# Performance work log

Measured on AMD Instinct MI355X. Metric: run time of the kernel, lower is better.

## Reference

```python
import jax, jax.numpy as jnp
import numpy as np
from functools import partial

H = 768
E = 1536
B = 4
L = 4096

def layer_norm(x, g, b, eps=1e-5):
    mu = jnp.mean(x, axis=-1, keepdims=True)
    var = jnp.mean((x - mu) ** 2, axis=-1, keepdims=True)
    return (x - mu) * jax.lax.rsqrt(var + eps) * g + b

def l2_normalize(x, eps=1e-12):
    n = jnp.sqrt(jnp.sum(x * x, axis=-1, keepdims=True))
    return x / jnp.maximum(n, eps)

def dw_conv(x, w):
    # x: [B, L, E], w: [E, 1, 3] depthwise kernel (torch Conv1d groups=E layout)
    y = jax.lax.conv_general_dilated(
        x.transpose(0, 2, 1), w, window_strides=(1,), padding=[(1, 1)],
        dimension_numbers=('NCH', 'OIH', 'NCH'), feature_group_count=E)
    return y.transpose(0, 2, 1)

def setup_inputs() -> dict:
    key = jax.random.key(0)
    ks = jax.random.split(key, 12)
    d = {}
    d['x'] = jax.random.normal(ks[0], (B, L, H), jnp.float32)
    d['ln1_g'] = jnp.ones((H,), jnp.float32)
    d['ln1_b'] = jnp.zeros((H,), jnp.float32)
    d['ln2_g'] = jnp.ones((E,), jnp.float32)
    d['ln2_b'] = jnp.zeros((E,), jnp.float32)
    d['W_in'] = 0.02 * jax.random.normal(ks[1], (3 * E, H), jnp.float32)
    d['b_in'] = jnp.zeros((3 * E,), jnp.float32)
    d['W_beta'] = jnp.zeros((E, H), jnp.float32)  # torch init: constant 0
    d['b_beta'] = jnp.ones((E,), jnp.float32)     # torch init: constant 1
    d['W_out'] = 0.02 * jax.random.normal(ks[2], (H, E), jnp.float32)
    d['b_out'] = jnp.zeros((H,), jnp.float32)
    d['W1'] = 0.02 * jax.random.normal(ks[3], (4 * H, H), jnp.float32)
    d['b1'] = jnp.zeros((4 * H,), jnp.float32)
    d['W2'] = 0.02 * jax.random.normal(ks[4], (H, 4 * H), jnp.float32)
    d['b2'] = jnp.zeros((H,), jnp.float32)
    d['conv_w'] = jax.random.normal(ks[5], (E, 1, 3), jnp.float32) / jnp.sqrt(3.0)
    d['attn_scale'] = jnp.ones((1,), jnp.float32)
    return d

def reference(x, ln1_g, ln1_b, ln2_g, ln2_b, W_in, b_in, W_beta, b_beta,
              W_out, b_out, W1, b1, W2, b2, conv_w, attn_scale):
    shortcut = x
    xn = layer_norm(x, ln1_g, ln1_b)
    qkv = xn @ W_in.T + b_in
    q, k, v = jnp.split(qkv, 3, axis=-1)
    q = jax.nn.silu(q)
    k = jax.nn.silu(k)
    v = jax.nn.gelu(v, approximate=False)
    q = l2_normalize(q) + 0.1 * k
    k = l2_normalize(k) + 0.1 * q
    q = dw_conv(q, conv_w)
    k = dw_conv(k, conv_w)
    v = dw_conv(v, conv_w)
    beta = jax.nn.sigmoid(xn @ W_beta.T + b_beta) * 0.9 + 0.1
    # initial state is zero, so v_old = 0 and v_new = beta * v (same math as torch code)
    v_new = beta * v                                   # [B, L, E]
    state = jnp.einsum('ble,blf->bef', v_new, k)       # v_new^T @ k : [B, E, E]
    out = jnp.einsum('blf,bef->ble', q, state)         # q @ state^T
    out = out * attn_scale
    out = layer_norm(out, ln2_g, ln2_b)
    out = out @ W_out.T + b_out
    x = shortcut + out
    h = layer_norm(x, ln1_g, ln1_b)
    h = jax.nn.gelu(h @ W1.T + b1, approximate=False) @ W2.T + b2
    return x + h
```

## Files before the change

kernel.cpp:

```cpp
#include <hip/hip_runtime.h>
#include <hip/hip_bf16.h>
#include <cstdint>
#include <cstddef>

using bf16_t = __hip_bfloat16;
typedef __bf16 bf16x8 __attribute__((ext_vector_type(8)));
typedef __bf16 bf16x4 __attribute__((ext_vector_type(4)));
typedef float f32x4 __attribute__((ext_vector_type(4)));

#define DEVI static __device__ __forceinline__

DEVI float b2f(bf16_t v) { return __bfloat162float(v); }

DEVI float fsigmoid(float x) { return 1.0f / (1.0f + __expf(-x)); }
DEVI float fsilu(float x) { return x * fsigmoid(x); }

DEVI float ferf(float x) {
    const float ax = fabsf(x);
    const float t = 1.0f / fmaf(0.3275911f, ax, 1.0f);
    float p = fmaf(1.061405429f, t, -1.453152027f);
    p = fmaf(p, t, 1.421413741f);
    p = fmaf(p, t, -0.284496736f);
    p = fmaf(p, t, 0.254829592f);
    p = p * t * __expf(-ax * ax);
    return copysignf(1.0f - p, x);
}
DEVI float fgelu(float x) { return 0.5f * x * (1.0f + ferf(x * 0.70710678118654752440f)); }

DEVI void g2l16(const bf16_t* g, bf16_t* l) {
    __builtin_amdgcn_global_load_lds(
        (const __attribute__((address_space(1))) void*)g,
        (__attribute__((address_space(3))) void*)l,
        16, 0, 0);
}

DEVI f32x4 mfma16(bf16x8 a, bf16x8 b, f32x4 c) {
    return __builtin_amdgcn_mfma_f32_16x16x32_bf16(a, b, c, 0, 0, 0);
}

template<int ACT, bool RESID, bool OUTBF, bool QKVSPLIT>
__global__ __launch_bounds__(256) void gemm_nt(
    const bf16_t* __restrict__ A, const bf16_t* __restrict__ B,
    void* __restrict__ Cout, const float* __restrict__ bias,
    const float* __restrict__ resid,
    float* __restrict__ normq, float* __restrict__ normk,
    int M, int N, int K, long long sA, long long sB, long long sC)
{
    __shared__ bf16_t As[128 * 64];
    __shared__ bf16_t Bs[128 * 64];

    const int t  = threadIdx.x;
    const int w  = t >> 6;
    const int ln = t & 63;
    const long long bz = blockIdx.z;
    A += bz * sA;
    B += bz * sB;
    const long long cbase = QKVSPLIT ? 0 : bz * sC;

    const int m0 = blockIdx.y * 128;
    const int n0 = blockIdx.x * 128;
    const int wm = (w >> 1) * 64;
    const int wn = (w & 1) * 64;

    f32x4 acc[4][4] = {};

    const int sr = ln >> 3;
    const int sc = (ln & 7) ^ sr;
    const bf16_t* Ap = A + (size_t)(m0 + w * 32 + sr) * K + sc * 8;
    const bf16_t* Bp = B + (size_t)(n0 + w * 32 + sr) * K + sc * 8;
    bf16_t* ldsA = &As[(w * 32) * 64];
    bf16_t* ldsB = &Bs[(w * 32) * 64];

    const int fr = ln & 15;
    const int qd = ln >> 4;
    int roA[4], roB[4];
#pragma unroll
    for (int i = 0; i < 4; ++i) {
        roA[i] = (wm + i * 16 + fr) * 64;
        roB[i] = (wn + i * 16 + fr) * 64;
    }
    const int so0 = ((qd)     ^ (fr & 7)) * 8;
    const int so1 = ((4 + qd) ^ (fr & 7)) * 8;

    for (int k0 = 0; k0 < K; k0 += 64) {
#pragma unroll
        for (int i = 0; i < 4; ++i) {
            g2l16(Ap + (size_t)(i * 8) * K, ldsA + (i * 8) * 64);
            g2l16(Bp + (size_t)(i * 8) * K, ldsB + (i * 8) * 64);
        }
        Ap += 64; Bp += 64;
        __syncthreads();

        bf16x8 af[4], bfr[4];
#pragma unroll
        for (int i = 0; i < 4; ++i) {
            af[i]  = *(const bf16x8*)&As[roA[i] + so0];
            bfr[i] = *(const bf16x8*)&Bs[roB[i] + so0];
        }
#pragma unroll
        for (int mi = 0; mi < 4; ++mi)
#pragma unroll
            for (int ni = 0; ni < 4; ++ni)
                acc[mi][ni] = mfma16(bfr[ni], af[mi], acc[mi][ni]);
#pragma unroll
        for (int i = 0; i < 4; ++i) {
            af[i]  = *(const bf16x8*)&As[roA[i] + so1];
            bfr[i] = *(const bf16x8*)&Bs[roB[i] + so1];
        }
#pragma unroll
        for (int mi = 0; mi < 4; ++mi)
#pragma unroll
            for (int ni = 0; ni < 4; ++ni)
                acc[mi][ni] = mfma16(bfr[ni], af[mi], acc[mi][ni]);
        __syncthreads();
    }

    const int rb = qd * 4;
    const int seg = QKVSPLIT ? (n0 / 1536) : 0;
    f32x4 bias4[4];
#pragma unroll
    for (int ni = 0; ni < 4; ++ni) {
        f32x4 z = {};
        bias4[ni] = bias ? *(const f32x4*)&bias[n0 + wn + ni * 16 + rb] : z;
    }
#pragma unroll
    for (int mi = 0; mi < 4; ++mi) {
        const int row = m0 + wm + mi * 16 + fr;
        float s2 = 0.f;
#pragma unroll
        for (int ni = 0; ni < 4; ++ni) {
            const int col0 = n0 + wn + ni * 16 + rb;
            f32x4 v = acc[mi][ni] + bias4[ni];
            if constexpr (ACT == 1) {
#pragma unroll
                for (int r = 0; r < 4; ++r) v[r] = fgelu(v[r]);
            }
            if constexpr (ACT == 3) {
                if (seg <= 1) {
#pragma unroll
                    for (int r = 0; r < 4; ++r) v[r] = fsilu(v[r]);
                    s2 += v[0]*v[0] + v[1]*v[1] + v[2]*v[2] + v[3]*v[3];
                } else if (seg == 2) {
#pragma unroll
                    for (int r = 0; r < 4; ++r) v[r] = fgelu(v[r]);
                } else {
#pragma unroll
                    for (int r = 0; r < 4; ++r) v[r] = fsigmoid(v[r]) * 0.9f + 0.1f;
                }
            }
            long long off;
            if constexpr (QKVSPLIT) {
                off = (long long)seg * sC + (long long)row * 1536
                    + (col0 - seg * 1536);
            } else {
                off = cbase + (long long)row * N + col0;
            }
            if constexpr (RESID) v += *(const f32x4*)&resid[off];
            if constexpr (OUTBF) {
                bf16x4 o;
#pragma unroll
                for (int r = 0; r < 4; ++r) o[r] = (__bf16)v[r];
                *(bf16x4*)((bf16_t*)Cout + off) = o;
            } else {
                *(f32x4*)((float*)Cout + off) = v;
            }
        }
        if constexpr (ACT == 3) {
            if (seg <= 1) {
                s2 += __shfl_xor(s2, 16, 64);
                s2 += __shfl_xor(s2, 32, 64);
                if (qd == 0)
                    atomicAdd((seg == 0 ? normq : normk) + row, s2);
            }
        }
    }
}

template<int ACT, bool RESID, bool OUTBF, bool QKVSPLIT>
__global__ __launch_bounds__(512) void gemm256(
    const bf16_t* __restrict__ A, const bf16_t* __restrict__ B,
    void* __restrict__ Cout, const float* __restrict__ bias,
    const float* __restrict__ resid,
    float* __restrict__ normq, float* __restrict__ normk,
    int M, int N, int K, long long sA, long long sB, long long sC)
{
    __shared__ bf16_t As[256 * 64];
    __shared__ bf16_t Bs[256 * 64];

    const int t  = threadIdx.x;
    const int w  = t >> 6;
    const int ln = t & 63;
    const int wr = w >> 2;
    const int wc = w & 3;
    const long long bz = blockIdx.z;
    A += bz * sA;
    B += bz * sB;
    const long long cbase = QKVSPLIT ? 0 : bz * sC;

    const int m0 = blockIdx.y * 256;
    const int n0 = blockIdx.x * 256;

    const int sr = ln >> 3;
    const int scx = ((ln & 7) ^ sr) * 8;
    const bf16_t* gA[2];
    const bf16_t* gB[2];
    int lA[2], lB[2];
#pragma unroll
    for (int i = 0; i < 2; ++i) {
        const int b  = w * 2 + i;
        const int rA = ((b >> 3) << 7) + ((b & 7) << 3);
        const int rB = ((b >> 2) << 6) + ((b & 3) << 3);
        gA[i] = A + (size_t)(m0 + rA + sr) * K + scx;
        gB[i] = B + (size_t)(n0 + rB + sr) * K + scx;
        lA[i] = rA * 64;
        lB[i] = rB * 64;
    }
    const size_t K64 = (size_t)K * 64;
    const size_t K32 = (size_t)K * 32;
    const int NT = K >> 6;

    const int fr = ln & 15;
    const int qd = ln >> 4;
    const int ck0 = ((qd)     ^ (fr & 7)) * 8;
    const int ck1 = ((4 + qd) ^ (fr & 7)) * 8;
    const int raB = (wr * 128 + fr) * 64;
    const int rbB = (wc * 64  + fr) * 64;

    f32x4 acc[8][4] = {};

#define STAGE_A0(kc) do { g2l16(gA[0] + (kc), &As[lA[0]]); \
                          g2l16(gA[1] + (kc), &As[lA[1]]); } while (0)
#define STAGE_A1(kc) do { g2l16(gA[0] + K64 + (kc), &As[lA[0] + 4096]); \
                          g2l16(gA[1] + K64 + (kc), &As[lA[1] + 4096]); } while (0)
#define STAGE_B0(kc) do { g2l16(gB[0] + (kc), &Bs[lB[0]]); \
                          g2l16(gB[1] + (kc), &Bs[lB[1]]); } while (0)
#define STAGE_B1(kc) do { g2l16(gB[0] + K32 + (kc), &Bs[lB[0] + 2048]); \
                          g2l16(gB[1] + K32 + (kc), &Bs[lB[1] + 2048]); } while (0)

    STAGE_A0(0);
    STAGE_B0(0);
    STAGE_B1(0);
    STAGE_A1(0);

    bf16x8 a0[4][2], a1[4][2], bq0[2][2], bq1[2][2];

    for (int u = 0; u < NT; ++u) {
        const size_t kc1 = (size_t)(u + 1) * 64;
        const bool p1 = (u + 1) < NT;

        asm volatile("s_waitcnt vmcnt(4)" ::: "memory");
        __builtin_amdgcn_sched_barrier(0);
        __builtin_amdgcn_s_barrier();
        __builtin_amdgcn_sched_barrier(0);
#pragma unroll
        for (int mi = 0; mi < 4; ++mi) {
            a0[mi][0] = *(const bf16x8*)&As[raB + mi * 1024 + ck0];
            a0[mi][1] = *(const bf16x8*)&As[raB + mi * 1024 + ck1];
        }
#pragma unroll
        for (int ni = 0; ni < 2; ++ni) {
            bq0[ni][0] = *(const bf16x8*)&Bs[rbB + ni * 1024 + ck0];
            bq0[ni][1] = *(const bf16x8*)&Bs[rbB + ni * 1024 + ck1];
        }
        asm volatile("s_waitcnt lgkmcnt(0)" ::: "memory");
        __builtin_amdgcn_sched_barrier(0);
        __builtin_amdgcn_s_setprio(1);
#pragma unroll
        for (int mi = 0; mi < 4; ++mi)
#pragma unroll
            for (int ni = 0; ni < 2; ++ni) {
                acc[mi][ni] = mfma16(bq0[ni][0], a0[mi][0], acc[mi][ni]);
                acc[mi][ni] = mfma16(bq0[ni][1], a0[mi][1], acc[mi][ni]);
            }
        __builtin_amdgcn_s_setprio(0);
        __builtin_amdgcn_sched_barrier(0);

        asm volatile("s_waitcnt vmcnt(2)" ::: "memory");
        __builtin_amdgcn_sched_barrier(0);
        __builtin_amdgcn_s_barrier();
        __builtin_amdgcn_sched_barrier(0);
        if (p1) STAGE_A0(kc1);
#pragma unroll
        for (int ni = 0; ni < 2; ++ni) {
            bq1[ni][0] = *(const bf16x8*)&Bs[rbB + 2048 + ni * 1024 + ck0];
            bq1[ni][1] = *(const bf16x8*)&Bs[rbB + 2048 + ni * 1024 + ck1];
        }
        asm volatile("s_waitcnt lgkmcnt(0)" ::: "memory");
        __builtin_amdgcn_sched_barrier(0);
        __builtin_amdgcn_s_setprio(1);
#pragma unroll
        for (int mi = 0; mi < 4; ++mi)
#pragma unroll
            for (int ni = 0; ni < 2; ++ni) {
                acc[mi][ni + 2] = mfma16(bq1[ni][0], a0[mi][0], acc[mi][ni + 2]);
                acc[mi][ni + 2] = mfma16(bq1[ni][1], a0[mi][1], acc[mi][ni + 2]);
            }
        __builtin_amdgcn_s_setprio(0);
        __builtin_amdgcn_sched_barrier(0);

        if (p1) asm volatile("s_waitcnt vmcnt(2)" ::: "memory");
        else    asm volatile("s_waitcnt vmcnt(0)" ::: "memory");
        __builtin_amdgcn_sched_barrier(0);
        __builtin_amdgcn_s_barrier();
        __builtin_amdgcn_sched_barrier(0);
        if (p1) { STAGE_B0(kc1); STAGE_B1(kc1); }
#pragma unroll
        for (int mi = 0; mi < 4; ++mi) {
            a1[mi][0] = *(const bf16x8*)&As[raB + 4096 + mi * 1024 + ck0];
            a1[mi][1] = *(const bf16x8*)&As[raB + 4096 + mi * 1024 + ck1];
        }
        asm volatile("s_waitcnt lgkmcnt(0)" ::: "memory");
        __builtin_amdgcn_sched_barrier(0);
        __builtin_amdgcn_s_setprio(1);
#pragma unroll
        for (int mi = 0; mi < 4; ++mi)
#pragma unroll
            for (int ni = 0; ni < 2; ++ni) {
                acc[mi + 4][ni] = mfma16(bq0[ni][0], a1[mi][0], acc[mi + 4][ni]);
                acc[mi + 4][ni] = mfma16(bq0[ni][1], a1[mi][1], acc[mi + 4][ni]);
            }
        __builtin_amdgcn_s_setprio(0);
        __builtin_amdgcn_sched_barrier(0);

        __builtin_amdgcn_s_barrier();
        __builtin_amdgcn_sched_barrier(0);
        if (p1) STAGE_A1(kc1);
        __builtin_amdgcn_s_setprio(1);
#pragma unroll
        for (int mi = 0; mi < 4; ++mi)
#pragma unroll
            for (int ni = 0; ni < 2; ++ni) {
                acc[mi + 4][ni + 2] = mfma16(bq1[ni][0], a1[mi][0], acc[mi + 4][ni + 2]);
                acc[mi + 4][ni + 2] = mfma16(bq1[ni][1], a1[mi][1], acc[mi + 4][ni + 2]);
            }
        __builtin_amdgcn_s_setprio(0);
        __builtin_amdgcn_sched_barrier(0);
    }
#undef STAGE_A0
#undef STAGE_A1
#undef STAGE_B0
#undef STAGE_B1

    const int rb = qd * 4;
    const int seg = QKVSPLIT ? (n0 / 1536) : 0;
    f32x4 bias4[4];
#pragma unroll
    for (int ni = 0; ni < 4; ++ni) {
        f32x4 z = {};
        bias4[ni] = bias ? *(const f32x4*)&bias[n0 + wc * 64 + ni * 16 + rb] : z;
    }
#pragma unroll
    for (int mi = 0; mi < 8; ++mi) {
        const int row = m0 + wr * 128 + mi * 16 + fr;
        float s2 = 0.f;
#pragma unroll
        for (int ni = 0; ni < 4; ++ni) {
            const int col0 = n0 + wc * 64 + ni * 16 + rb;
            f32x4 v = acc[mi][ni] + bias4[ni];
            if constexpr (ACT == 1) {
#pragma unroll
                for (int r = 0; r < 4; ++r) v[r] = fgelu(v[r]);
            }
            if constexpr (ACT == 3) {
                if (seg <= 1) {
#pragma unroll
                    for (int r = 0; r < 4; ++r) v[r] = fsilu(v[r]);
                    s2 += v[0]*v[0] + v[1]*v[1] + v[2]*v[2] + v[3]*v[3];
                } else if (seg == 2) {
#pragma unroll
                    for (int r = 0; r < 4; ++r) v[r] = fgelu(v[r]);
                } else {
#pragma unroll
                    for (int r = 0; r < 4; ++r) v[r] = fsigmoid(v[r]) * 0.9f + 0.1f;
                }
            }
            long long off;
            if constexpr (QKVSPLIT) {
                off = (long long)seg * sC + (long long)row * 1536
                    + (col0 - seg * 1536);
            } else {
                off = cbase + (long long)row * N + col0;
            }
            if constexpr (RESID) v += *(const f32x4*)&resid[off];
            if constexpr (OUTBF) {
                bf16x4 o;
#pragma unroll
                for (int r = 0; r < 4; ++r) o[r] = (__bf16)v[r];
                *(bf16x4*)((bf16_t*)Cout + off) = o;
            } else {
                *(f32x4*)((float*)Cout + off) = v;
            }
        }
        if constexpr (ACT == 3) {
            if (seg <= 1) {
                s2 += __shfl_xor(s2, 16, 64);
                s2 += __shfl_xor(s2, 32, 64);
                if (qd == 0)
                    atomicAdd((seg == 0 ? normq : normk) + row, s2);
            }
        }
    }
}

template<int NT>
__global__ __launch_bounds__(NT) void ln_v4(
    const float* __restrict__ x, const float* __restrict__ g,
    const float* __restrict__ b, bf16_t* __restrict__ out)
{
    constexpr int n = NT * 4;
    constexpr int NW = NT / 64;
    const int row = blockIdx.x, t = threadIdx.x;
    f32x4 v = *(const f32x4*)&x[(size_t)row * n + t * 4];
    float s  = v[0] + v[1] + v[2] + v[3];
    float ss = v[0]*v[0] + v[1]*v[1] + v[2]*v[2] + v[3]*v[3];
#pragma unroll
    for (int m = 32; m; m >>= 1) { s += __shfl_xor(s, m, 64); ss += __shfl_xor(ss, m, 64); }
    __shared__ float red[2 * NW];
    const int w = t >> 6;
    if ((t & 63) == 0) { red[w] = s; red[NW + w] = ss; }
    __syncthreads();
    s = 0.f; ss = 0.f;
#pragma unroll
    for (int i = 0; i < NW; ++i) { s += red[i]; ss += red[NW + i]; }
    const float mean = s / n;
    const float rstd = rsqrtf(ss / n - mean * mean + 1e-5f);
    const f32x4 gv = *(const f32x4*)&g[t * 4];
    const f32x4 bv = *(const f32x4*)&b[t * 4];
    bf16x4 o;
#pragma unroll
    for (int r = 0; r < 4; ++r)
        o[r] = (__bf16)((v[r] - mean) * rstd * gv[r] + bv[r]);
    *(bf16x4*)&out[(size_t)row * n + t * 4] = o;
}

__global__ __launch_bounds__(192) void ln_bf16_1536(
    const bf16_t* __restrict__ x, const float* __restrict__ g,
    const float* __restrict__ b, bf16_t* __restrict__ out,
    const float* __restrict__ scale_ptr)
{
    const int row = blockIdx.x, t = threadIdx.x;
    const float scale = scale_ptr[0];
    const bf16x8 x8 = *(const bf16x8*)&x[(size_t)row * 1536 + t * 8];
    float v[8];
    float s = 0.f, ss = 0.f;
#pragma unroll
    for (int i = 0; i < 8; ++i) {
        v[i] = (float)x8[i] * scale;
        s += v[i]; ss += v[i] * v[i];
    }
#pragma unroll
    for (int m = 32; m; m >>= 1) { s += __shfl_xor(s, m, 64); ss += __shfl_xor(ss, m, 64); }
    __shared__ float red[6];
    const int w = t >> 6;
    if ((t & 63) == 0) { red[w] = s; red[3 + w] = ss; }
    __syncthreads();
    s  = red[0] + red[1] + red[2];
    ss = red[3] + red[4] + red[5];
    const float mean = s / 1536.f;
    const float rstd = rsqrtf(ss / 1536.f - mean * mean + 1e-5f);
    const f32x4 g0 = *(const f32x4*)&g[t * 8];
    const f32x4 g1 = *(const f32x4*)&g[t * 8 + 4];
    const f32x4 b0 = *(const f32x4*)&b[t * 8];
    const f32x4 b1 = *(const f32x4*)&b[t * 8 + 4];
    bf16x8 o;
#pragma unroll
    for (int r = 0; r < 4; ++r) {
        o[r]     = (__bf16)((v[r]     - mean) * rstd * g0[r] + b0[r]);
        o[r + 4] = (__bf16)((v[r + 4] - mean) * rstd * g1[r] + b1[r]);
    }
    *(bf16x8*)&out[(size_t)row * 1536 + t * 8] = o;
}

__global__ __launch_bounds__(256) void ac_qk(
    const bf16_t* __restrict__ qs, const bf16_t* __restrict__ ks,
    const float* __restrict__ nq, const float* __restrict__ nk,
    bf16_t* __restrict__ qc, bf16_t* __restrict__ kT,
    const float* __restrict__ cw)
{
    constexpr int L = 4096, E = 1536;
    const int b = blockIdx.z;
    const int e0 = blockIdx.x * 64, l0 = blockIdx.y * 64;
    const int t = threadIdx.x;
    const int e = e0 + (t & 15) * 4;
    const int lbase = l0 + (t >> 4) * 4;
    const size_t rowL = (size_t)b * L;

    float w0[4], w1[4], w2[4];
#pragma unroll
    for (int i = 0; i < 4; ++i) {
        w0[i] = cw[(e + i) * 3 + 0];
        w1[i] = cw[(e + i) * 3 + 1];
        w2[i] = cw[(e + i) * 3 + 2];
    }

    float sq[6][4], sk[6][4];
#pragma unroll
    for (int j = 0; j < 6; ++j) {
        const int l = lbase - 1 + j;
        if (l < 0 || l >= L) {
#pragma unroll
            for (int i = 0; i < 4; ++i) { sq[j][i] = 0.f; sk[j][i] = 0.f; }
            continue;
        }
        const size_t off = (rowL + l) * E + e;
        const bf16x4 q4 = *(const bf16x4*)&qs[off];
        const bf16x4 k4 = *(const bf16x4*)&ks[off];
        const float rq = 1.0f / fmaxf(sqrtf(nq[rowL + l]), 1e-12f);
        const float rk = 1.0f / fmaxf(sqrtf(nk[rowL + l]), 1e-12f);
#pragma unroll
        for (int i = 0; i < 4; ++i) {
            const float q1 = (float)q4[i] * rq + 0.1f * (float)k4[i];
            const float k1 = (float)k4[i] * rk + 0.1f * q1;
            sq[j][i] = q1; sk[j][i] = k1;
        }
    }

#pragma unroll
    for (int j = 0; j < 4; ++j) {
        bf16x4 oq;
#pragma unroll
        for (int i = 0; i < 4; ++i)
            oq[i] = (__bf16)(w0[i] * sq[j][i] + w1[i] * sq[j + 1][i] + w2[i] * sq[j + 2][i]);
        *(bf16x4*)&qc[(rowL + lbase + j) * E + e] = oq;
    }
#pragma unroll
    for (int i = 0; i < 4; ++i) {
        bf16x4 ok;
#pragma unroll
        for (int j = 0; j < 4; ++j)
            ok[j] = (__bf16)(w0[i] * sk[j][i] + w1[i] * sk[j + 1][i] + w2[i] * sk[j + 2][i]);
        *(bf16x4*)&kT[((size_t)b * E + e + i) * L + lbase] = ok;
    }
}

__global__ __launch_bounds__(256) void ac_v(
    const bf16_t* __restrict__ vg, const bf16_t* __restrict__ beta,
    bf16_t* __restrict__ vT, const float* __restrict__ cw)
{
    constexpr int L = 4096, E = 1536;
    const int b = blockIdx.z;
    const int e0 = blockIdx.x * 64, l0 = blockIdx.y * 64;
    const int t = threadIdx.x;
    const int e = e0 + (t & 15) * 4;
    const int lbase = l0 + (t >> 4) * 4;
    const size_t rowL = (size_t)b * L;

    float w0[4], w1[4], w2[4];
#pragma unroll
    for (int i = 0; i < 4; ++i) {
        w0[i] = cw[(e + i) * 3 + 0];
        w1[i] = cw[(e + i) * 3 + 1];
        w2[i] = cw[(e + i) * 3 + 2];
    }

    float s[6][4];
#pragma unroll
    for (int j = 0; j < 6; ++j) {
        const int l = lbase - 1 + j;
        if (l < 0 || l >= L) {
#pragma unroll
            for (int i = 0; i < 4; ++i) s[j][i] = 0.f;
            continue;
        }
        const bf16x4 v4 = *(const bf16x4*)&vg[(rowL + l) * E + e];
#pragma unroll
        for (int i = 0; i < 4; ++i) s[j][i] = (float)v4[i];
    }

    float o[4][4];
#pragma unroll
    for (int j = 0; j < 4; ++j) {
        const bf16x4 b4 = *(const bf16x4*)&beta[(rowL + lbase + j) * E + e];
#pragma unroll
        for (int i = 0; i < 4; ++i)
            o[j][i] = (w0[i] * s[j][i] + w1[i] * s[j + 1][i] + w2[i] * s[j + 2][i])
                      * (float)b4[i];
    }
#pragma unroll
    for (int i = 0; i < 4; ++i) {
        bf16x4 ov;
#pragma unroll
        for (int j = 0; j < 4; ++j) ov[j] = (__bf16)o[j][i];
        *(bf16x4*)&vT[((size_t)b * E + e + i) * L + lbase] = ov;
    }
}

__global__ __launch_bounds__(256) void prep1(
    const float* __restrict__ Win, const float* __restrict__ Wbeta,
    const float* __restrict__ bin, const float* __restrict__ bbeta,
    bf16_t* __restrict__ Wcat, float* __restrict__ bcat)
{
    constexpr int nWin4 = 3 * 1536 * 768 / 4;
    constexpr int nWb4  = 1536 * 768 / 4;
    const int i = blockIdx.x * 256 + threadIdx.x;
    if (i < nWin4) {
        const f32x4 v = ((const f32x4*)Win)[i];
        bf16x4 o;
#pragma unroll
        for (int r = 0; r < 4; ++r) o[r] = (__bf16)v[r];
        ((bf16x4*)Wcat)[i] = o;
    } else if (i < nWin4 + nWb4) {
        const f32x4 v = ((const f32x4*)Wbeta)[i - nWin4];
        bf16x4 o;
#pragma unroll
        for (int r = 0; r < 4; ++r) o[r] = (__bf16)v[r];
        ((bf16x4*)Wcat)[i] = o;
    } else {
        const int j = i - nWin4 - nWb4;
        ((f32x4*)bcat)[j] = (j < 1152) ? ((const f32x4*)bin)[j]
                                       : ((const f32x4*)bbeta)[j - 1152];
    }
}

__global__ __launch_bounds__(256) void prep2(
    const float* __restrict__ Wout, const float* __restrict__ W1,
    const float* __restrict__ W2, bf16_t* __restrict__ dst)
{
    constexpr int n0 = 768 * 1536 / 4;
    constexpr int n1 = n0 + 3072 * 768 / 4;
    const int i = blockIdx.x * 256 + threadIdx.x;
    const float* src;
    int j;
    if (i < n0)      { src = Wout; j = i; }
    else if (i < n1) { src = W1;   j = i - n0; }
    else             { src = W2;   j = i - n1; }
    const f32x4 v = ((const f32x4*)src)[j];
    bf16x4 o;
#pragma unroll
    for (int r = 0; r < 4; ++r) o[r] = (__bf16)v[r];
    ((bf16x4*)dst)[i] = o;
}

__global__ void diag_ws(float* o, float v) { o[threadIdx.x] = v; }


extern "C" void kernel_launch(void* const* d_in, const int* in_sizes, int n_in,
                              void* d_out, int out_size, void* d_ws, size_t ws_size,
                              hipStream_t stream)
{
    constexpr int B = 4, L = 4096, H = 768, E = 1536;
    constexpr int T = B * L;
    constexpr size_t SEGE = (size_t)T * E;
    constexpr size_t S    = SEGE * 2;
    constexpr size_t o_bcat  = 5 * S;
    constexpr size_t o_norms = o_bcat + 6144 * 4;
    constexpr size_t WS_NEED = o_norms + (size_t)T * 8;

    const float* x       = (const float*)d_in[0];
    const float* ln1_g   = (const float*)d_in[1];
    const float* ln1_b   = (const float*)d_in[2];
    const float* ln2_g   = (const float*)d_in[3];
    const float* ln2_b   = (const float*)d_in[4];
    const float* W_in    = (const float*)d_in[5];
    const float* b_in    = (const float*)d_in[6];
    const float* W_beta  = (const float*)d_in[7];
    const float* b_beta  = (const float*)d_in[8];
    const float* W_out   = (const float*)d_in[9];
    const float* b_out   = (const float*)d_in[10];
    const float* W1      = (const float*)d_in[11];
    const float* b1      = (const float*)d_in[12];
    const float* W2      = (const float*)d_in[13];
    const float* b2      = (const float*)d_in[14];
    const float* conv_w  = (const float*)d_in[15];
    const float* attn_sc = (const float*)d_in[16];

    if (ws_size < WS_NEED) {
        diag_ws<<<1, 256, 0, stream>>>((float*)d_out,
                                       10000.0f + (float)(ws_size >> 20));
        return;
    }

    char* ws = (char*)d_ws;
    bf16_t* slotA = (bf16_t*)(ws + 0 * S);
    bf16_t* slotB = (bf16_t*)(ws + 1 * S);
    bf16_t* slotC = (bf16_t*)(ws + 2 * S);
    bf16_t* slotD = (bf16_t*)(ws + 3 * S);
    bf16_t* slotE = (bf16_t*)(ws + 4 * S);
    float*  bcat  = (float*)(ws + o_bcat);
    float*  nq    = (float*)(ws + o_norms);
    float*  nk    = nq + T;

    bf16_t* Wcat = slotE;
    bf16_t* xn   = (bf16_t*)((char*)slotE + (size_t)6144 * H * 2);

    bf16_t* vT    = slotE;
    bf16_t* kT    = slotC;
    bf16_t* qc    = slotD;
    bf16_t* state = slotA;
    bf16_t* WoutB = (bf16_t*)((char*)slotA + (size_t)20 * 1024 * 1024);
    bf16_t* W1B   = WoutB + (size_t)H * E;
    bf16_t* W2B   = W1B + (size_t)4 * H * H;
    bf16_t* attn  = slotB;
    bf16_t* ln2o  = slotE;
    float*  x2    = (float*)slotC;
    bf16_t* xn2   = slotB;
    bf16_t* h1    = slotD;

    hipMemsetAsync(nq, 0, (size_t)T * 2 * sizeof(float), stream);
    prep1<<<4614, 256, 0, stream>>>(W_in, W_beta, b_in, b_beta, Wcat, bcat);

    ln_v4<192><<<T, 192, 0, stream>>>(x, ln1_g, ln1_b, xn);

    gemm256<3, false, true, true><<<dim3(6144 / 256, T / 256, 1), 512, 0, stream>>>(
        xn, Wcat, slotA, bcat, nullptr, nq, nk, T, 6144, H, 0, 0, (long long)SEGE);

    ac_v <<<dim3(E / 64, L / 64, B), 256, 0, stream>>>(slotC, slotD, vT, conv_w);
    ac_qk<<<dim3(E / 64, L / 64, B), 256, 0, stream>>>(slotA, slotB, nq, nk, qc, kT, conv_w);

    prep2<<<5760, 256, 0, stream>>>(W_out, W1, W2, WoutB);

    gemm_nt<0, false, true, false><<<dim3(E / 128, E / 128, B), 256, 0, stream>>>(
        vT, kT, state, nullptr, nullptr, nullptr, nullptr, E, E, L,
        (long long)E * L, (long long)E * L, (long long)E * E);

    gemm256<0, false, true, false><<<dim3(E / 256, L / 256, B), 512, 0, stream>>>(
        qc, state, attn, nullptr, nullptr, nullptr, nullptr, L, E, E,
        (long long)L * E, (long long)E * E, (long long)L * E);

    ln_bf16_1536<<<T, 192, 0, stream>>>(attn, ln2_g, ln2_b, ln2o, attn_sc);

    gemm_nt<0, true, false, false><<<dim3(H / 128, T / 128, 1), 256, 0, stream>>>(
        ln2o, WoutB, x2, b_out, x, nullptr, nullptr, T, H, E, 0, 0, 0);

    ln_v4<192><<<T, 192, 0, stream>>>(x2, ln1_g, ln1_b, xn2);

    gemm256<1, false, true, false><<<dim3(4 * H / 256, T / 256, 1), 512, 0, stream>>>(
        xn2, W1B, h1, b1, nullptr, nullptr, nullptr, T, 4 * H, H, 0, 0, 0);

    gemm_nt<0, true, false, false><<<dim3(H / 128, T / 128, 1), 256, 0, stream>>>(
        h1, W2B, (float*)d_out, b2, x2, nullptr, nullptr, T, H, 4 * H, 0, 0, 0);
}
```

Measured before the change: 1.150 ms.

## Double-buffer LDS tiles in gemm256 with two-half k-step pipeline

Replaces the single-buffered four-phase staging schedule with ping-pong LDS buffers for A and B. The next tile's A loads are issued at the top of each iteration and its B loads are issued mid-iteration, while the current tile is consumed in two k-halves of 8x4 MFMAs each. The aim is to cut the number of workgroup barriers per k-step and overlap global-to-LDS copies with compute more fully. In exchange, LDS use doubles to 128KB, which may limit occupancy, and more fragment registers are live at once.

```diff
diff --git a/kernel.cpp b/kernel.cpp
--- a/kernel.cpp
+++ b/kernel.cpp
@@ -184,8 +184,8 @@
     float* __restrict__ normq, float* __restrict__ normk,
     int M, int N, int K, long long sA, long long sB, long long sC)
 {
-    __shared__ bf16_t As[256 * 64];
-    __shared__ bf16_t Bs[256 * 64];
+    __shared__ bf16_t As[2][256 * 64];
+    __shared__ bf16_t Bs[2][256 * 64];
 
     const int t  = threadIdx.x;
     const int w  = t >> 6;
@@ -223,123 +223,87 @@
     const int qd = ln >> 4;
     const int ck0 = ((qd)     ^ (fr & 7)) * 8;
     const int ck1 = ((4 + qd) ^ (fr & 7)) * 8;
-    const int raB = (wr * 128 + fr) * 64;
-    const int rbB = (wc * 64  + fr) * 64;
+    int roA[8], roB[4];
+#pragma unroll
+    for (int mi = 0; mi < 8; ++mi) roA[mi] = (wr * 128 + mi * 16 + fr) * 64;
+#pragma unroll
+    for (int ni = 0; ni < 4; ++ni) roB[ni] = (wc * 64 + ni * 16 + fr) * 64;
 
     f32x4 acc[8][4] = {};
 
-#define STAGE_A0(kc) do { g2l16(gA[0] + (kc), &As[lA[0]]); \
-                          g2l16(gA[1] + (kc), &As[lA[1]]); } while (0)
-#define STAGE_A1(kc) do { g2l16(gA[0] + K64 + (kc), &As[lA[0] + 4096]); \
-                          g2l16(gA[1] + K64 + (kc), &As[lA[1] + 4096]); } while (0)
-#define STAGE_B0(kc) do { g2l16(gB[0] + (kc), &Bs[lB[0]]); \
-                          g2l16(gB[1] + (kc), &Bs[lB[1]]); } while (0)
-#define STAGE_B1(kc) do { g2l16(gB[0] + K32 + (kc), &Bs[lB[0] + 2048]); \
-                          g2l16(gB[1] + K32 + (kc), &Bs[lB[1] + 2048]); } while (0)
-
-    STAGE_A0(0);
-    STAGE_B0(0);
-    STAGE_B1(0);
-    STAGE_A1(0);
-
-    bf16x8 a0[4][2], a1[4][2], bq0[2][2], bq1[2][2];
+#define STAGE_A(dst, kc) do { \
+    g2l16(gA[0] + (kc),       &(dst)[lA[0]]); \
+    g2l16(gA[0] + K64 + (kc), &(dst)[lA[0] + 4096]); \
+    g2l16(gA[1] + (kc),       &(dst)[lA[1]]); \
+    g2l16(gA[1] + K64 + (kc), &(dst)[lA[1] + 4096]); } while (0)
+#define STAGE_B(dst, kc) do { \
+    g2l16(gB[0] + (kc),       &(dst)[lB[0]]); \
+    g2l16(gB[0] + K32 + (kc), &(dst)[lB[0] + 2048]); \
+    g2l16(gB[1] + (kc),       &(dst)[lB[1]]); \
+    g2l16(gB[1] + K32 + (kc), &(dst)[lB[1] + 2048]); } while (0)
+
+    STAGE_A(As[0], 0);
+    STAGE_B(Bs[0], 0);
 
     for (int u = 0; u < NT; ++u) {
+        const bf16_t* Ac = As[u & 1];
+        const bf16_t* Bc = Bs[u & 1];
+        bf16_t* An = As[(u + 1) & 1];
+        bf16_t* Bn = Bs[(u + 1) & 1];
         const size_t kc1 = (size_t)(u + 1) * 64;
         const bool p1 = (u + 1) < NT;
 
-        asm volatile("s_waitcnt vmcnt(4)" ::: "memory");
-        __builtin_amdgcn_sched_barrier(0);
+        if (p1) {
+            STAGE_A(An, kc1);
+            asm volatile("s_waitcnt vmcnt(4)" ::: "memory");
+        } else {
+            asm volatile("s_waitcnt vmcnt(0)" ::: "memory");
+        }
         __builtin_amdgcn_s_barrier();
         __builtin_amdgcn_sched_barrier(0);
-#pragma unroll
-        for (int mi = 0; mi < 4; ++mi) {
-            a0[mi][0] = *(const bf16x8*)&As[raB + mi * 1024 + ck0];
-            a0[mi][1] = *(const bf16x8*)&As[raB + mi * 1024 + ck1];
-        }
-#pragma unroll
-        for (int ni = 0; ni < 2; ++ni) {
-            bq0[ni][0] = *(const bf16x8*)&Bs[rbB + ni * 1024 + ck0];
-            bq0[ni][1] = *(const bf16x8*)&Bs[rbB + ni * 1024 + ck1];
-        }
-        asm volatile("s_waitcnt lgkmcnt(0)" ::: "memory");
-        __builtin_amdgcn_sched_barrier(0);
-        __builtin_amdgcn_s_setprio(1);
-#pragma unroll
-        for (int mi = 0; mi < 4; ++mi)
-#pragma unroll
-            for (int ni = 0; ni < 2; ++ni) {
-                acc[mi][ni] = mfma16(bq0[ni][0], a0[mi][0], acc[mi][ni]);
-                acc[mi][ni] = mfma16(bq0[ni][1], a0[mi][1], acc[mi][ni]);
-            }
-        __builtin_amdgcn_s_setprio(0);
-        __builtin_amdgcn_sched_barrier(0);
-
-        asm volatile("s_waitcnt vmcnt(2)" ::: "memory");
-        __builtin_amdgcn_sched_barrier(0);
-        __builtin_amdgcn_s_barrier();
-        __builtin_amdgcn_sched_barrier(0);
-        if (p1) STAGE_A0(kc1);
-#pragma unroll
-        for (int ni = 0; ni < 2; ++ni) {
-            bq1[ni][0] = *(const bf16x8*)&Bs[rbB + 2048 + ni * 1024 + ck0];
-            bq1[ni][1] = *(const bf16x8*)&Bs[rbB + 2048 + ni * 1024 + ck1];
-        }
-        asm volatile("s_waitcnt lgkmcnt(0)" ::: "memory");
-        __builtin_amdgcn_sched_barrier(0);
-        __builtin_amdgcn_s_setprio(1);
-#pragma unroll
-        for (int mi = 0; mi < 4; ++mi)
-#pragma unroll
-            for (int ni = 0; ni < 2; ++ni) {
-                acc[mi][ni + 2] = mfma16(bq1[ni][0], a0[mi][0], acc[mi][ni + 2]);
-                acc[mi][ni + 2] = mfma16(bq1[ni][1], a0[mi][1], acc[mi][ni + 2]);
-            }
-        __builtin_amdgcn_s_setprio(0);
-        __builtin_amdgcn_sched_barrier(0);
-
-        if (p1) asm volatile("s_waitcnt vmcnt(2)" ::: "memory");
-        else    asm volatile("s_waitcnt vmcnt(0)" ::: "memory");
-        __builtin_amdgcn_sched_barrier(0);
-        __builtin_amdgcn_s_barrier();
-        __builtin_amdgcn_sched_barrier(0);
-        if (p1) { STAGE_B0(kc1); STAGE_B1(kc1); }
-#pragma unroll
-        for (int mi = 0; mi < 4; ++mi) {
-            a1[mi][0] = *(const bf16x8*)&As[raB + 4096 + mi * 1024 + ck0];
-            a1[mi][1] = *(const bf16x8*)&As[raB + 4096 + mi * 1024 + ck1];
-        }
-        asm volatile("s_waitcnt lgkmcnt(0)" ::: "memory");
-        __builtin_amdgcn_sched_barrier(0);
-        __builtin_amdgcn_s_setprio(1);
-#pragma unroll
-        for (int mi = 0; mi < 4; ++mi)
-#pragma unroll
-            for (int ni = 0; ni < 2; ++ni) {
-                acc[mi + 4][ni] = mfma16(bq0[ni][0], a1[mi][0], acc[mi + 4][ni]);
-                acc[mi + 4][ni] = mfma16(bq0[ni][1], a1[mi][1], acc[mi + 4][ni]);
-            }
-        __builtin_amdgcn_s_setprio(0);
-        __builtin_amdgcn_sched_barrier(0);
-
-        __builtin_amdgcn_s_barrier();
-        __builtin_amdgcn_sched_barrier(0);
-        if (p1) STAGE_A1(kc1);
-        __builtin_amdgcn_s_setprio(1);
-#pragma unroll
-        for (int mi = 0; mi < 4; ++mi)
-#pragma unroll
-            for (int ni = 0; ni < 2; ++ni) {
-                acc[mi + 4][ni + 2] = mfma16(bq1[ni][0], a1[mi][0], acc[mi + 4][ni + 2]);
-                acc[mi + 4][ni + 2] = mfma16(bq1[ni][1], a1[mi][1], acc[mi + 4][ni + 2]);
-            }
-        __builtin_amdgcn_s_setprio(0);
-        __builtin_amdgcn_sched_barrier(0);
-    }
-#undef STAGE_A0
-#undef STAGE_A1
-#undef STAGE_B0
-#undef STAGE_B1
+        {
+            bf16x8 af[8], bfr[4];
+#pragma unroll
+            for (int mi = 0; mi < 8; ++mi)
+                af[mi] = *(const bf16x8*)&Ac[roA[mi] + ck0];
+#pragma unroll
+            for (int ni = 0; ni < 4; ++ni)
+                bfr[ni] = *(const bf16x8*)&Bc[roB[ni] + ck0];
+            __builtin_amdgcn_s_setprio(1);
+#pragma unroll
+            for (int mi = 0; mi < 8; ++mi)
+#pragma unroll
+                for (int ni = 0; ni < 4; ++ni)
+                    acc[mi][ni] = mfma16(bfr[ni], af[mi], acc[mi][ni]);
+            __builtin_amdgcn_s_setprio(0);
+        }
+
+        if (p1) STAGE_B(Bn, kc1);
+        {
+            bf16x8 af[8], bfr[4];
+#pragma unroll
+            for (int mi = 0; mi < 8; ++mi)
+                af[mi] = *(const bf16x8*)&Ac[roA[mi] + ck1];
+#pragma unroll
+            for (int ni = 0; ni < 4; ++ni)
+                bfr[ni] = *(const bf16x8*)&Bc[roB[ni] + ck1];
+            __builtin_amdgcn_s_setprio(1);
+#pragma unroll
+            for (int mi = 0; mi < 8; ++mi)
+#pragma unroll
+                for (int ni = 0; ni < 4; ++ni)
+                    acc[mi][ni] = mfma16(bfr[ni], af[mi], acc[mi][ni]);
+            __builtin_amdgcn_s_setprio(0);
+        }
+
+        if (p1) {
+            asm volatile("s_waitcnt vmcnt(4)" ::: "memory");
+            __builtin_amdgcn_s_barrier();
+            __builtin_amdgcn_sched_barrier(0);
+        }
+    }
+#undef STAGE_A
+#undef STAGE_B
 
     const int rb = qd * 4;
     const int seg = QKVSPLIT ? (n0 / 1536) : 0;
```

After: 1.013 ms. 1.14x faster.
